# Kernel optimization log

Hardware: AMD Instinct MI355X
Metric: run time of the kernel (lower is better)

Reference implementation:

```python
import jax, jax.numpy as jnp
from jax import lax
import numpy as np

NUM_KIND = 4
V, H, B = 34, 32, 4096   # raw vertical (2 rows dropped), horizontal, batch
KS = 33                  # odd-rounded max(V-2, H)
NUM_DEPTH = 4
N_SQ = 100


def _conv(x, w):
    # x: (N,1,h,w), w: (1,1,KS,KS); torch Conv2d == cross-correlation == lax default
    return lax.conv_general_dilated(x, w, (1, 1), 'SAME',
                                    dimension_numbers=('NCHW', 'OIHW', 'NCHW'))


def _conv_k(x, w):
    # x: (K,B,1,h,w) -> conv each map with the shared 1-channel kernel
    k, b, c, h, wd = x.shape
    return _conv(x.reshape(k * b, c, h, wd), w).reshape(k, b, c, h, wd)


def setup_inputs() -> dict:
    key = jax.random.key(0)
    ks = jax.random.split(key, 8)
    std = 0.3
    return {
        'dots':    jax.random.randint(ks[0], (V, H, B), 0, NUM_KIND + 1, dtype=jnp.int32),
        'w_each':  jax.random.normal(ks[1], (1, 1, KS, KS), jnp.float32) * std,
        'w_not':   jax.random.normal(ks[2], (1, 1, KS, KS), jnp.float32) * std,
        'w_not2':  jax.random.normal(ks[3], (1, 1, KS, KS), jnp.float32) * std,
        'w_empty': jax.random.normal(ks[4], (1, 1, KS, KS), jnp.float32) * std,
        'W1':      jax.random.normal(ks[5], (N_SQ, (V - 2) * H), jnp.float32) * std,
        'W2':      jax.random.normal(ks[6], (N_SQ, N_SQ), jnp.float32) * std,
        'W3':      jax.random.normal(ks[7], (1, N_SQ), jnp.float32) * std,
    }


def reference(dots, w_each, w_not, w_not2, w_empty, W1, W2, W3):
    # drop last 2 vertical rows, layout (V-2,H,B) -> (B,1,V-2,H)
    board = dots[:-2].astype(jnp.float32).transpose(2, 0, 1)[:, None]  # (B,1,h,w)

    empty = (board == 0).astype(jnp.float32)
    E = _conv(empty, w_empty)                                           # (B,1,h,w)

    kinds = jnp.arange(1, NUM_KIND + 1, dtype=board.dtype).reshape(NUM_KIND, 1, 1, 1, 1)
    each = (board[None] == kinds).astype(jnp.float32)                   # (K,B,1,h,w)
    notm = ((each + empty[None]) == 0).astype(jnp.float32)              # (K,B,1,h,w)

    # first pass: per-color value, masked to that color's cells
    notm_conv = _conv_k(notm, w_not)      # note: the torch code LOGS the convolved not-mask
    v = _conv_k(each, w_each) + E[None] - notm_conv
    L = each * v                          # each_color_value_log (masked)
    s = jax.nn.sigmoid(L.sum(axis=0))     # all_color_value_2nd, (B,1,h,w)

    # iterative diffusion; torch mutates the log in-place each depth:
    # L <- mask * (L + E + conv2nd(notm_conv * before)); before is detached
    for _ in range(NUM_DEPTH):
        before = lax.stop_gradient(s)
        C = _conv_k(notm_conv * before[None], w_not2)
        L = each * (L + E[None] + C)
        s = jax.nn.sigmoid(L.sum(axis=0))

    feat = s.reshape(s.shape[0], -1)      # (B, (V-2)*H)
    x = jax.nn.leaky_relu(feat @ W1.T, 0.2)
    x = jax.nn.leaky_relu(x @ W2.T, 0.2)
    return x @ W3.T                        # (B,1)
```

## Files before the change

### kernel.cpp

```cpp
#include <hip/hip_runtime.h>
#include <cstdint>
#include <cstddef>


typedef _Float16 f16;
typedef __attribute__((ext_vector_type(8))) _Float16 f16x8;
typedef __attribute__((ext_vector_type(4))) float f32x4;

#define NB   4096
#define PIX  1024
#define MR   (NB * 4)

__device__ __forceinline__ void gld_lds16(const void* g, void* l) {
    __builtin_amdgcn_global_load_lds(
        (const __attribute__((address_space(1))) void*)g,
        (__attribute__((address_space(3))) void*)l, 16, 0, 0);
}

__global__ void build_all(const float* __restrict__ we, const float* __restrict__ wn,
                          const float* __restrict__ wn2, const float* __restrict__ wem,
                          const float* __restrict__ W1, const int* __restrict__ dots,
                          f16* __restrict__ Me, f16* __restrict__ Mn,
                          f16* __restrict__ Mn2, f16* __restrict__ Mem,
                          f16* __restrict__ W1b, unsigned char* __restrict__ board) {
    __shared__ unsigned char tile[64][68];
    int bi = blockIdx.x, t = threadIdx.x;
    if (bi < 4096) {
        int idx = bi * 256 + t;
        int o = idx >> 10, in = idx & 1023;
        int i = o >> 5, j = o & 31, a = in >> 5, b = in & 31;
        int u = a - i + 16, v = b - j + 16;
        bool ok = (u >= 0) && (u < 33) && (v >= 0) && (v < 33);
        int w = u * 33 + v;
        float ve = 0.f, vn = 0.f, vn2 = 0.f, vem = 0.f;
        if (ok) { ve = we[w]; vn = wn[w]; vn2 = wn2[w]; vem = wem[w]; }
        Me[idx]  = (f16)ve;
        Mn[idx]  = (f16)vn;
        Mn2[idx] = (f16)vn2;
        Mem[idx] = (f16)vem;
    } else if (bi < 4608) {
        int idx = (bi - 4096) * 256 + t;
        int j = idx >> 10, i = idx & 1023;
        W1b[idx] = (f16)(j < 100 ? W1[j * 1024 + i] : 0.f);
    } else {
        int bb = bi - 4608;
        int bp = bb & 15, bn = bb >> 4;
        int p0 = bp * 64, n0 = bn * 64;
        int ln = t & 63, lp = t >> 6;
#pragma unroll
        for (int j = 0; j < 16; j++) {
            int p = lp * 16 + j;
            tile[p][ln] = (unsigned char)dots[(size_t)(p0 + p) * 4096 + n0 + ln];
        }
        __syncthreads();
#pragma unroll
        for (int j = 0; j < 16; j++) {
            int n = lp * 16 + j;
            board[(size_t)(n0 + n) * 1024 + p0 + ln] = tile[ln][n];
        }
    }
}

template <int MODE, int ASRC>
__device__ __forceinline__ void run_gemm(
    int bjob, int ypx, int nx, char* smem,
    const f16* __restrict__ X, const f16* __restrict__ B,
    const unsigned char* __restrict__ board, const f16* __restrict__ En,
    const f16* __restrict__ NCs, f16* __restrict__ Lsel,
    f16* __restrict__ Pout, f16* __restrict__ outB, int ldo) {
    char* smB = smem;
    char* smA = smem + 16384;

    const int tid = threadIdx.x;
    const int wv = tid >> 6, ln = tid & 63;
    const int wm = wv >> 1, wn_ = wv & 1;
    const int lr = ln & 15, lq = ln >> 4;

    int xcd = bjob & 7, slot = bjob >> 3;
    int bx = slot % nx;
    int by = xcd * ypx + slot / nx;
    const int rtile = by * 128, otile = bx * 128;
    const int img0 = (ASRC == 4) ? rtile : (rtile >> 2);

    const f32x4 fz = {0.f, 0.f, 0.f, 0.f};
    f32x4 acc[4][4];
#pragma unroll
    for (int i = 0; i < 4; i++)
#pragma unroll
        for (int j = 0; j < 4; j++) acc[i][j] = fz;

    for (int kb = 0; kb < 1024; kb += 64) {
#pragma unroll
        for (int t = 0; t < 4; t++) {
            int c = (wv * 4 + t) * 64 + ln;
            int row = c >> 3, gcol = (c & 7) ^ (row & 7);
            gld_lds16(B + (size_t)(otile + row) * 1024 + kb + gcol * 8, smB + c * 16);
        }
        if (ASRC == 0) {
#pragma unroll
            for (int t = 0; t < 4; t++) {
                int c = (wv * 4 + t) * 64 + ln;
                int row = c >> 3, gcol = (c & 7) ^ (row & 7);
                gld_lds16(X + (size_t)(rtile + row) * 1024 + kb + gcol * 8, smA + c * 16);
            }
        } else if (ASRC == 4) {
#pragma unroll
            for (int t = 0; t < 2; t++) {
                int c = t * 256 + wv * 64 + ln;
                int row = c >> 2, g = (c & 3) ^ (row & 3);
                gld_lds16(board + (size_t)(img0 + row) * 1024 + kb + g * 16, smA + c * 16);
            }
        } else {
            if (wv < 2) {
                int c = wv * 64 + ln;
                int row = c >> 2, g = (c & 3) ^ (row & 3);
                gld_lds16(board + (size_t)(img0 + row) * 1024 + kb + g * 16, smA + c * 16);
            }
        }
        __syncthreads();

#pragma unroll
        for (int kk = 0; kk < 2; kk++) {
            const int oct = kk * 4 + lq;
            f16x8 af[4], bfr[4];
#pragma unroll
            for (int i = 0; i < 4; i++) {
                int rrow = wm * 64 + i * 16 + lr;
                if (ASRC == 0) {
                    af[i] = *(const f16x8*)(smA + rrow * 128 + (oct ^ (rrow & 7)) * 16);
                } else {
                    int m = (ASRC == 4) ? rrow : (rrow >> 2);
                    int k1 = (rrow & 3) + 1;
                    uint64_t bb = *(const uint64_t*)(smA + m * 64 +
                                    ((oct >> 1) ^ (m & 3)) * 16 + (oct & 1) * 8);
                    f16x8 v;
#pragma unroll
                    for (int jj = 0; jj < 8; jj++) {
                        int bj = (int)((bb >> (8 * jj)) & 0xff);
                        bool on = (ASRC == 2) ? (bj == k1)
                                : (ASRC == 3) ? (bj != 0 && bj != k1)
                                              : (bj == 0);
                        v[jj] = on ? (f16)1.f : (f16)0.f;
                    }
                    af[i] = v;
                }
            }
#pragma unroll
            for (int j = 0; j < 4; j++) {
                int brow = wn_ * 64 + j * 16 + lr;
                bfr[j] = *(const f16x8*)(smB + brow * 128 + (oct ^ (brow & 7)) * 16);
            }
#pragma unroll
            for (int i = 0; i < 4; i++)
#pragma unroll
                for (int j = 0; j < 4; j++)
                    acc[i][j] = __builtin_amdgcn_mfma_f32_16x16x32_f16(
                        af[i], bfr[j], acc[i][j], 0, 0, 0);
        }
        __syncthreads();
    }

#pragma unroll
    for (int i = 0; i < 4; i++) {
        int rbase = rtile + wm * 64 + i * 16 + lq * 4;
#pragma unroll
        for (int j = 0; j < 4; j++) {
            int o = otile + wn_ * 64 + j * 16 + lr;
            f32x4 a = acc[i][j];
            if (MODE == 0) {
#pragma unroll
                for (int v = 0; v < 4; v++)
                    outB[(size_t)(rbase + v) * ldo + o] = (f16)a[v];
            } else {
                int n = rbase >> 2;
                size_t no = (size_t)n * PIX + o;
                int c = board[no];
                float asel = (c == 1) ? a[0] : (c == 2) ? a[1] : (c == 3) ? a[2] : a[3];
                size_t r0 = (size_t)rbase * PIX + o;
                f16 nc0 = NCs[r0], nc1 = NCs[r0 + PIX];
                f16 nc2 = NCs[r0 + 2 * PIX], nc3 = NCs[r0 + 3 * PIX];
                float L = 0.f;
                if (c > 0) {
                    float ncsel = (float)((c == 1) ? nc0 : (c == 2) ? nc1
                                        : (c == 3) ? nc2 : nc3);
                    L = asel + (float)En[no] - ncsel;
                }
                Lsel[no] = (f16)L;
                f16 s = (f16)(1.f / (1.f + __expf(-L)));
                Pout[r0]           = nc0 * s;
                Pout[r0 + PIX]     = nc1 * s;
                Pout[r0 + 2 * PIX] = nc2 * s;
                Pout[r0 + 3 * PIX] = nc3 * s;
            }
        }
    }
}

__global__ void __launch_bounds__(256, 4) gemm_faA(
    const f16* __restrict__ Mn, const f16* __restrict__ Mem,
    const unsigned char* __restrict__ board,
    f16* __restrict__ NC, f16* __restrict__ En) {
    __shared__ __attribute__((aligned(16))) char smem[24576];
    int bi = blockIdx.x;
    if (bi < 1024) {
        run_gemm<0, 3>(bi, 16, 8, smem, nullptr, Mn, board, nullptr, nullptr,
                       nullptr, nullptr, NC, PIX);
    } else {
        run_gemm<0, 4>(bi - 1024, 4, 8, smem, nullptr, Mem, board, nullptr, nullptr,
                       nullptr, nullptr, En, PIX);
    }
}

__global__ void __launch_bounds__(256, 4) gemm_faB(
    const f16* __restrict__ Me, const unsigned char* __restrict__ board,
    const f16* __restrict__ En, const f16* __restrict__ NC,
    f16* __restrict__ Lsel, f16* __restrict__ P1) {
    __shared__ __attribute__((aligned(16))) char smem[24576];
    run_gemm<2, 2>(blockIdx.x, 16, 8, smem, nullptr, Me, board, En, NC,
                   Lsel, P1, nullptr, 0);
}

template <int MODE>
__global__ void __launch_bounds__(256, 2) gemm_depth(
    const f16* __restrict__ Pin, const f16* __restrict__ Mn2,
    const unsigned char* __restrict__ board, const f16* __restrict__ NC,
    const f16* __restrict__ En, f16* __restrict__ Lsel,
    f16* __restrict__ Pout, f16* __restrict__ feat) {
    __shared__ __attribute__((aligned(16))) char smem[32768];
    char* smB = smem;
    char* smA = smem + 16384;

    const int tid = threadIdx.x;
    const int wv = tid >> 6, ln = tid & 63;
    const int wm = wv >> 1, wn_ = wv & 1;
    const int lr = ln & 15, lq = ln >> 4;

    int bi = blockIdx.x;
    int xcd = bi & 7, slot = bi >> 3;
    int bx = slot & 7;
    int by = xcd * 16 + (slot >> 3);
    const int rtile = by * 128, otile = bx * 128;

    const f32x4 fz = {0.f, 0.f, 0.f, 0.f};
    f32x4 acc[4][4];
#pragma unroll
    for (int i = 0; i < 4; i++)
#pragma unroll
        for (int j = 0; j < 4; j++) acc[i][j] = fz;

    for (int kb = 0; kb < 1024; kb += 64) {
#pragma unroll
        for (int t = 0; t < 4; t++) {
            int c = (wv * 4 + t) * 64 + ln;
            int row = c >> 3, gcol = (c & 7) ^ (row & 7);
            gld_lds16(Mn2 + (size_t)(otile + row) * 1024 + kb + gcol * 8, smB + c * 16);
            gld_lds16(Pin + (size_t)(rtile + row) * 1024 + kb + gcol * 8, smA + c * 16);
        }
        __syncthreads();

#pragma unroll
        for (int kk = 0; kk < 2; kk++) {
            const int oct = kk * 4 + lq;
            f16x8 af[4], bfr[4];
#pragma unroll
            for (int i = 0; i < 4; i++) {
                int rrow = wm * 64 + i * 16 + lr;
                af[i] = *(const f16x8*)(smA + rrow * 128 + (oct ^ (rrow & 7)) * 16);
            }
#pragma unroll
            for (int j = 0; j < 4; j++) {
                int brow = wn_ * 64 + j * 16 + lr;
                bfr[j] = *(const f16x8*)(smB + brow * 128 + (oct ^ (brow & 7)) * 16);
            }
#pragma unroll
            for (int i = 0; i < 4; i++)
#pragma unroll
                for (int j = 0; j < 4; j++)
                    acc[i][j] = __builtin_amdgcn_mfma_f32_16x16x32_f16(
                        af[i], bfr[j], acc[i][j], 0, 0, 0);
        }
        __syncthreads();
    }

#pragma unroll
    for (int i = 0; i < 4; i++) {
        int rbase = rtile + wm * 64 + i * 16 + lq * 4;
#pragma unroll
        for (int j = 0; j < 4; j++) {
            int o = otile + wn_ * 64 + j * 16 + lr;
            f32x4 a = acc[i][j];
            int n = rbase >> 2;
            size_t no = (size_t)n * PIX + o;
            int c = board[no];
            float asel = (c == 1) ? a[0] : (c == 2) ? a[1] : (c == 3) ? a[2] : a[3];
            float E = (float)En[no];
            float Lnew = (c > 0) ? ((float)Lsel[no] + E + asel) : 0.f;
            float s = 1.f / (1.f + __expf(-Lnew));
            if (MODE == 4) {
                feat[no] = (f16)s;
            } else {
                Lsel[no] = (f16)Lnew;
                f16 sh = (f16)s;
                size_t r0 = (size_t)rbase * PIX + o;
                Pout[r0]           = NC[r0] * sh;
                Pout[r0 + PIX]     = NC[r0 + PIX] * sh;
                Pout[r0 + 2 * PIX] = NC[r0 + 2 * PIX] * sh;
                Pout[r0 + 3 * PIX] = NC[r0 + 3 * PIX] * sh;
            }
        }
    }
}

__global__ void __launch_bounds__(256) gemm_mlp_fused(
    const f16* __restrict__ feat, const f16* __restrict__ W1b,
    const float* __restrict__ W2, const float* __restrict__ W3,
    float* __restrict__ out) {
    __shared__ __attribute__((aligned(16))) char smem[47360];
    char* smB = smem;
    char* smA = smem + 16384;

    const int tid = threadIdx.x;
    const int wv = tid >> 6, ln = tid & 63;
    const int wm = wv >> 1, wn_ = wv & 1;
    const int lr = ln & 15, lq = ln >> 4;
    const int rtile = blockIdx.x * 128;

    const f32x4 fz = {0.f, 0.f, 0.f, 0.f};
    f32x4 acc[4][4];
#pragma unroll
    for (int i = 0; i < 4; i++)
#pragma unroll
        for (int j = 0; j < 4; j++) acc[i][j] = fz;

    for (int kb = 0; kb < 1024; kb += 64) {
#pragma unroll
        for (int t = 0; t < 4; t++) {
            int c = (wv * 4 + t) * 64 + ln;
            int row = c >> 3, gcol = (c & 7) ^ (row & 7);
            gld_lds16(W1b  + (size_t)row * 1024 + kb + gcol * 8, smB + c * 16);
            gld_lds16(feat + (size_t)(rtile + row) * 1024 + kb + gcol * 8, smA + c * 16);
        }
        __syncthreads();
#pragma unroll
        for (int kk = 0; kk < 2; kk++) {
            const int oct = kk * 4 + lq;
            f16x8 af[4], bfr[4];
#pragma unroll
            for (int i = 0; i < 4; i++) {
                int rrow = wm * 64 + i * 16 + lr;
                af[i] = *(const f16x8*)(smA + rrow * 128 + (oct ^ (rrow & 7)) * 16);
            }
#pragma unroll
            for (int j = 0; j < 4; j++) {
                int brow = wn_ * 64 + j * 16 + lr;
                bfr[j] = *(const f16x8*)(smB + brow * 128 + (oct ^ (brow & 7)) * 16);
            }
#pragma unroll
            for (int i = 0; i < 4; i++)
#pragma unroll
                for (int j = 0; j < 4; j++)
                    acc[i][j] = __builtin_amdgcn_mfma_f32_16x16x32_f16(
                        af[i], bfr[j], acc[i][j], 0, 0, 0);
        }
        __syncthreads();
    }

    float* xs  = (float*)smem;
    f16*   sW2 = (f16*)(smem + 25856);
    float* sW3 = (float*)(smem + 45856);
    float* red = (float*)(smem + 46272);
    for (int idx = tid; idx < 10000; idx += 256) sW2[idx] = (f16)W2[idx];
    if (tid < 100) sW3[tid] = W3[tid];

    for (int half = 0; half < 2; half++) {
        if (wm == half) {
#pragma unroll
            for (int i = 0; i < 4; i++) {
                int rb = i * 16 + lq * 4;
#pragma unroll
                for (int j = 0; j < 4; j++) {
                    int o = wn_ * 64 + j * 16 + lr;
                    if (o < 100) {
                        f32x4 a = acc[i][j];
#pragma unroll
                        for (int v = 0; v < 4; v++) {
                            float x = a[v];
                            xs[(rb + v) * 101 + o] = x > 0.f ? x : 0.2f * x;
                        }
                    }
                }
            }
        }
        __syncthreads();
        int nb = tid >> 2, q = tid & 3;
        const float* xrow = xs + nb * 101;
        float partial = 0.f;
        for (int jj = 0; jj < 25; jj++) {
            int j = q + jj * 4;
            const f16* w2r = sW2 + j * 100;
            float a2 = 0.f;
#pragma unroll
            for (int i = 0; i < 100; i++) a2 += (float)w2r[i] * xrow[i];
            partial += sW3[j] * (a2 > 0.f ? a2 : 0.2f * a2);
        }
        red[tid] = partial;
        __syncthreads();
        if (q == 0)
            out[rtile + half * 64 + nb] = red[tid] + red[tid + 1] + red[tid + 2] + red[tid + 3];
        __syncthreads();
    }
}

extern "C" void kernel_launch(void* const* d_in, const int* in_sizes, int n_in,
                              void* d_out, int out_size, void* d_ws, size_t ws_size,
                              hipStream_t stream) {
    (void)in_sizes; (void)n_in; (void)out_size; (void)ws_size;
    const int*   dots   = (const int*)d_in[0];
    const float* w_each = (const float*)d_in[1];
    const float* w_not  = (const float*)d_in[2];
    const float* w_not2 = (const float*)d_in[3];
    const float* w_emp  = (const float*)d_in[4];
    const float* W1 = (const float*)d_in[5];
    const float* W2 = (const float*)d_in[6];
    const float* W3 = (const float*)d_in[7];
    float* out = (float*)d_out;

    char* ws = (char*)d_ws;
    size_t off = 0;
    auto alloc = [&](size_t bytes) -> char* {
        char* p = ws + off;
        off += (bytes + 255) & ~(size_t)255;
        return p;
    };
    f16* Me    = (f16*)alloc((size_t)PIX * PIX * 2);
    f16* Mn    = (f16*)alloc((size_t)PIX * PIX * 2);
    f16* Mn2   = (f16*)alloc((size_t)PIX * PIX * 2);
    f16* Mem   = (f16*)alloc((size_t)PIX * PIX * 2);
    f16* W1b   = (f16*)alloc((size_t)128 * PIX * 2);
    unsigned char* board = (unsigned char*)alloc((size_t)NB * PIX);
    f16* NC    = (f16*)alloc((size_t)MR * PIX * 2);
    f16* En    = (f16*)alloc((size_t)NB * PIX * 2);
    f16* Pa    = (f16*)alloc((size_t)MR * PIX * 2);
    f16* Pb    = (f16*)alloc((size_t)MR * PIX * 2);
    f16* feat  = (f16*)alloc((size_t)NB * PIX * 2);
    f16* Lsel  = (f16*)alloc((size_t)NB * PIX * 2);

    dim3 blk(256);
    build_all<<<5632, blk, 0, stream>>>(w_each, w_not, w_not2, w_emp, W1, dots,
                                        Me, Mn, Mn2, Mem, W1b, board);
    gemm_faA<<<1280, blk, 0, stream>>>(Mn, Mem, board, NC, En);
    gemm_faB<<<1024, blk, 0, stream>>>(Me, board, En, NC, Lsel, Pa);
    gemm_depth<3><<<1024, blk, 0, stream>>>(Pa, Mn2, board, NC, En, Lsel, Pb, nullptr);
    gemm_depth<3><<<1024, blk, 0, stream>>>(Pb, Mn2, board, NC, En, Lsel, Pa, nullptr);
    gemm_depth<3><<<1024, blk, 0, stream>>>(Pa, Mn2, board, NC, En, Lsel, Pb, nullptr);
    gemm_depth<4><<<1024, blk, 0, stream>>>(Pb, Mn2, board, NC, En, Lsel, nullptr, feat);
    gemm_mlp_fused<<<32, blk, 0, stream>>>(feat, W1b, W2, W3, out);
}
```

Baseline: 409.4 us.

## Precompute f16 masks and fuse sigmoid-times-notconv product into depth GEMM operand load

Adds an expand_masks kernel that writes the per-kind each, not and empty masks as f16 matrices once, so the first-pass GEMMs load plain f16 A tiles instead of decoding board bytes per MFMA fragment. The depth GEMMs no longer read a precomputed P = NC*s buffer (4 values per pixel written in every epilogue). They load NC and the per-image sigmoid S tile into LDS and multiply them while building the A fragments. Each epilogue then writes only Lsel and S per pixel. The cost is extra mask buffers, the extra expansion pass, one more LDS tile and a vector multiply in the inner loop.

```diff
diff --git a/kernel.cpp b/kernel.cpp
--- a/kernel.cpp
+++ b/kernel.cpp
@@ -61,13 +61,43 @@
     }
 }
 
-template <int MODE, int ASRC>
+__global__ void expand_masks(const unsigned char* __restrict__ board,
+                             f16* __restrict__ eachF, f16* __restrict__ notmF,
+                             f16* __restrict__ emptyF) {
+    int bi = blockIdx.x, t = threadIdx.x;
+    if (bi < 8192) {
+        int idx = bi * 256 + t;
+        int r = idx >> 7, w0 = (idx & 127) << 3;
+        int n = r >> 2, k1 = (r & 3) + 1;
+        uint64_t bb = *(const uint64_t*)(board + (size_t)n * 1024 + w0);
+        f16x8 e, m;
+#pragma unroll
+        for (int j = 0; j < 8; j++) {
+            int bj = (int)((bb >> (8 * j)) & 0xff);
+            e[j] = (bj == k1) ? (f16)1.f : (f16)0.f;
+            m[j] = (bj != 0 && bj != k1) ? (f16)1.f : (f16)0.f;
+        }
+        *(f16x8*)(eachF + (size_t)idx * 8) = e;
+        *(f16x8*)(notmF + (size_t)idx * 8) = m;
+    } else {
+        int idx = (bi - 8192) * 256 + t;
+        int n = idx >> 7, w0 = (idx & 127) << 3;
+        uint64_t bb = *(const uint64_t*)(board + (size_t)n * 1024 + w0);
+        f16x8 e;
+#pragma unroll
+        for (int j = 0; j < 8; j++)
+            e[j] = (((bb >> (8 * j)) & 0xff) == 0) ? (f16)1.f : (f16)0.f;
+        *(f16x8*)(emptyF + (size_t)idx * 8) = e;
+    }
+}
+
+template <int MODE>
 __device__ __forceinline__ void run_gemm(
     int bjob, int ypx, int nx, char* smem,
     const f16* __restrict__ X, const f16* __restrict__ B,
     const unsigned char* __restrict__ board, const f16* __restrict__ En,
     const f16* __restrict__ NCs, f16* __restrict__ Lsel,
-    f16* __restrict__ Pout, f16* __restrict__ outB, int ldo) {
+    f16* __restrict__ Sout, f16* __restrict__ outB, int ldo) {
     char* smB = smem;
     char* smA = smem + 16384;
 
@@ -80,7 +110,6 @@
     int bx = slot % nx;
     int by = xcd * ypx + slot / nx;
     const int rtile = by * 128, otile = bx * 128;
-    const int img0 = (ASRC == 4) ? rtile : (rtile >> 2);
 
     const f32x4 fz = {0.f, 0.f, 0.f, 0.f};
     f32x4 acc[4][4];
@@ -95,27 +124,7 @@
             int c = (wv * 4 + t) * 64 + ln;
             int row = c >> 3, gcol = (c & 7) ^ (row & 7);
             gld_lds16(B + (size_t)(otile + row) * 1024 + kb + gcol * 8, smB + c * 16);
-        }
-        if (ASRC == 0) {
-#pragma unroll
-            for (int t = 0; t < 4; t++) {
-                int c = (wv * 4 + t) * 64 + ln;
-                int row = c >> 3, gcol = (c & 7) ^ (row & 7);
-                gld_lds16(X + (size_t)(rtile + row) * 1024 + kb + gcol * 8, smA + c * 16);
-            }
-        } else if (ASRC == 4) {
-#pragma unroll
-            for (int t = 0; t < 2; t++) {
-                int c = t * 256 + wv * 64 + ln;
-                int row = c >> 2, g = (c & 3) ^ (row & 3);
-                gld_lds16(board + (size_t)(img0 + row) * 1024 + kb + g * 16, smA + c * 16);
-            }
-        } else {
-            if (wv < 2) {
-                int c = wv * 64 + ln;
-                int row = c >> 2, g = (c & 3) ^ (row & 3);
-                gld_lds16(board + (size_t)(img0 + row) * 1024 + kb + g * 16, smA + c * 16);
-            }
+            gld_lds16(X + (size_t)(rtile + row) * 1024 + kb + gcol * 8, smA + c * 16);
         }
         __syncthreads();
 
@@ -126,24 +135,7 @@
 #pragma unroll
             for (int i = 0; i < 4; i++) {
                 int rrow = wm * 64 + i * 16 + lr;
-                if (ASRC == 0) {
-                    af[i] = *(const f16x8*)(smA + rrow * 128 + (oct ^ (rrow & 7)) * 16);
-                } else {
-                    int m = (ASRC == 4) ? rrow : (rrow >> 2);
-                    int k1 = (rrow & 3) + 1;
-                    uint64_t bb = *(const uint64_t*)(smA + m * 64 +
-                                    ((oct >> 1) ^ (m & 3)) * 16 + (oct & 1) * 8);
-                    f16x8 v;
-#pragma unroll
-                    for (int jj = 0; jj < 8; jj++) {
-                        int bj = (int)((bb >> (8 * jj)) & 0xff);
-                        bool on = (ASRC == 2) ? (bj == k1)
-                                : (ASRC == 3) ? (bj != 0 && bj != k1)
-                                              : (bj == 0);
-                        v[jj] = on ? (f16)1.f : (f16)0.f;
-                    }
-                    af[i] = v;
-                }
+                af[i] = *(const f16x8*)(smA + rrow * 128 + (oct ^ (rrow & 7)) * 16);
             }
 #pragma unroll
             for (int j = 0; j < 4; j++) {
@@ -175,22 +167,15 @@
                 int n = rbase >> 2;
                 size_t no = (size_t)n * PIX + o;
                 int c = board[no];
-                float asel = (c == 1) ? a[0] : (c == 2) ? a[1] : (c == 3) ? a[2] : a[3];
-                size_t r0 = (size_t)rbase * PIX + o;
-                f16 nc0 = NCs[r0], nc1 = NCs[r0 + PIX];
-                f16 nc2 = NCs[r0 + 2 * PIX], nc3 = NCs[r0 + 3 * PIX];
                 float L = 0.f;
                 if (c > 0) {
-                    float ncsel = (float)((c == 1) ? nc0 : (c == 2) ? nc1
-                                        : (c == 3) ? nc2 : nc3);
+                    float asel = (c == 1) ? a[0] : (c == 2) ? a[1]
+                               : (c == 3) ? a[2] : a[3];
+                    float ncsel = (float)NCs[(size_t)(rbase + c - 1) * PIX + o];
                     L = asel + (float)En[no] - ncsel;
                 }
                 Lsel[no] = (f16)L;
-                f16 s = (f16)(1.f / (1.f + __expf(-L)));
-                Pout[r0]           = nc0 * s;
-                Pout[r0 + PIX]     = nc1 * s;
-                Pout[r0 + 2 * PIX] = nc2 * s;
-                Pout[r0 + 3 * PIX] = nc3 * s;
+                Sout[no] = (f16)(1.f / (1.f + __expf(-L)));
             }
         }
     }
@@ -198,37 +183,37 @@
 
 __global__ void __launch_bounds__(256, 4) gemm_faA(
     const f16* __restrict__ Mn, const f16* __restrict__ Mem,
-    const unsigned char* __restrict__ board,
+    const f16* __restrict__ notmF, const f16* __restrict__ emptyF,
     f16* __restrict__ NC, f16* __restrict__ En) {
-    __shared__ __attribute__((aligned(16))) char smem[24576];
+    __shared__ __attribute__((aligned(16))) char smem[32768];
     int bi = blockIdx.x;
     if (bi < 1024) {
-        run_gemm<0, 3>(bi, 16, 8, smem, nullptr, Mn, board, nullptr, nullptr,
-                       nullptr, nullptr, NC, PIX);
+        run_gemm<0>(bi, 16, 8, smem, notmF, Mn, nullptr, nullptr,
+                    nullptr, nullptr, nullptr, NC, PIX);
     } else {
-        run_gemm<0, 4>(bi - 1024, 4, 8, smem, nullptr, Mem, board, nullptr, nullptr,
-                       nullptr, nullptr, En, PIX);
+        run_gemm<0>(bi - 1024, 4, 8, smem, emptyF, Mem, nullptr, nullptr,
+                    nullptr, nullptr, nullptr, En, PIX);
     }
 }
 
 __global__ void __launch_bounds__(256, 4) gemm_faB(
-    const f16* __restrict__ Me, const unsigned char* __restrict__ board,
-    const f16* __restrict__ En, const f16* __restrict__ NC,
-    f16* __restrict__ Lsel, f16* __restrict__ P1) {
-    __shared__ __attribute__((aligned(16))) char smem[24576];
-    run_gemm<2, 2>(blockIdx.x, 16, 8, smem, nullptr, Me, board, En, NC,
-                   Lsel, P1, nullptr, 0);
-}
-
-template <int MODE>
+    const f16* __restrict__ Me, const f16* __restrict__ eachF,
+    const unsigned char* __restrict__ board, const f16* __restrict__ En,
+    const f16* __restrict__ NC, f16* __restrict__ Lsel, f16* __restrict__ S1) {
+    __shared__ __attribute__((aligned(16))) char smem[32768];
+    run_gemm<2>(blockIdx.x, 16, 8, smem, eachF, Me, board, En, NC,
+                Lsel, S1, nullptr, 0);
+}
+
 __global__ void __launch_bounds__(256, 2) gemm_depth(
-    const f16* __restrict__ Pin, const f16* __restrict__ Mn2,
-    const unsigned char* __restrict__ board, const f16* __restrict__ NC,
-    const f16* __restrict__ En, f16* __restrict__ Lsel,
-    f16* __restrict__ Pout, f16* __restrict__ feat) {
-    __shared__ __attribute__((aligned(16))) char smem[32768];
+    const f16* __restrict__ NC, const f16* __restrict__ Mn2,
+    const unsigned char* __restrict__ board, const f16* __restrict__ En,
+    const f16* __restrict__ Sin, f16* __restrict__ Lsel,
+    f16* __restrict__ Sout) {
+    __shared__ __attribute__((aligned(16))) char smem[36864];
     char* smB = smem;
     char* smA = smem + 16384;
+    char* smS = smem + 32768;
 
     const int tid = threadIdx.x;
     const int wv = tid >> 6, ln = tid & 63;
@@ -240,6 +225,7 @@
     int bx = slot & 7;
     int by = xcd * 16 + (slot >> 3);
     const int rtile = by * 128, otile = bx * 128;
+    const int n0 = rtile >> 2;
 
     const f32x4 fz = {0.f, 0.f, 0.f, 0.f};
     f32x4 acc[4][4];
@@ -254,7 +240,11 @@
             int c = (wv * 4 + t) * 64 + ln;
             int row = c >> 3, gcol = (c & 7) ^ (row & 7);
             gld_lds16(Mn2 + (size_t)(otile + row) * 1024 + kb + gcol * 8, smB + c * 16);
-            gld_lds16(Pin + (size_t)(rtile + row) * 1024 + kb + gcol * 8, smA + c * 16);
+            gld_lds16(NC  + (size_t)(rtile + row) * 1024 + kb + gcol * 8, smA + c * 16);
+        }
+        {
+            int row = tid >> 3, col = tid & 7;
+            gld_lds16(Sin + (size_t)(n0 + row) * 1024 + kb + col * 8, smS + tid * 16);
         }
         __syncthreads();
 
@@ -265,7 +255,9 @@
 #pragma unroll
             for (int i = 0; i < 4; i++) {
                 int rrow = wm * 64 + i * 16 + lr;
-                af[i] = *(const f16x8*)(smA + rrow * 128 + (oct ^ (rrow & 7)) * 16);
+                f16x8 nv = *(const f16x8*)(smA + rrow * 128 + (oct ^ (rrow & 7)) * 16);
+                f16x8 sv = *(const f16x8*)(smS + (rrow >> 2) * 128 + oct * 16);
+                af[i] = nv * sv;
             }
 #pragma unroll
             for (int j = 0; j < 4; j++) {
@@ -292,21 +284,14 @@
             int n = rbase >> 2;
             size_t no = (size_t)n * PIX + o;
             int c = board[no];
-            float asel = (c == 1) ? a[0] : (c == 2) ? a[1] : (c == 3) ? a[2] : a[3];
-            float E = (float)En[no];
-            float Lnew = (c > 0) ? ((float)Lsel[no] + E + asel) : 0.f;
-            float s = 1.f / (1.f + __expf(-Lnew));
-            if (MODE == 4) {
-                feat[no] = (f16)s;
-            } else {
-                Lsel[no] = (f16)Lnew;
-                f16 sh = (f16)s;
-                size_t r0 = (size_t)rbase * PIX + o;
-                Pout[r0]           = NC[r0] * sh;
-                Pout[r0 + PIX]     = NC[r0 + PIX] * sh;
-                Pout[r0 + 2 * PIX] = NC[r0 + 2 * PIX] * sh;
-                Pout[r0 + 3 * PIX] = NC[r0 + 3 * PIX] * sh;
-            }
+            float Lnew = 0.f;
+            if (c > 0) {
+                float asel = (c == 1) ? a[0] : (c == 2) ? a[1]
+                           : (c == 3) ? a[2] : a[3];
+                Lnew = (float)Lsel[no] + (float)En[no] + asel;
+            }
+            Lsel[no] = (f16)Lnew;
+            Sout[no] = (f16)(1.f / (1.f + __expf(-Lnew)));
         }
     }
 }
@@ -438,21 +423,24 @@
     f16* Mem   = (f16*)alloc((size_t)PIX * PIX * 2);
     f16* W1b   = (f16*)alloc((size_t)128 * PIX * 2);
     unsigned char* board = (unsigned char*)alloc((size_t)NB * PIX);
+    f16* eachF = (f16*)alloc((size_t)MR * PIX * 2);
+    f16* notmF = (f16*)alloc((size_t)MR * PIX * 2);
+    f16* emptyF= (f16*)alloc((size_t)NB * PIX * 2);
     f16* NC    = (f16*)alloc((size_t)MR * PIX * 2);
     f16* En    = (f16*)alloc((size_t)NB * PIX * 2);
-    f16* Pa    = (f16*)alloc((size_t)MR * PIX * 2);
-    f16* Pb    = (f16*)alloc((size_t)MR * PIX * 2);
-    f16* feat  = (f16*)alloc((size_t)NB * PIX * 2);
     f16* Lsel  = (f16*)alloc((size_t)NB * PIX * 2);
+    f16* Sa    = (f16*)alloc((size_t)NB * PIX * 2);
+    f16* Sb    = (f16*)alloc((size_t)NB * PIX * 2);
 
     dim3 blk(256);
     build_all<<<5632, blk, 0, stream>>>(w_each, w_not, w_not2, w_emp, W1, dots,
                                         Me, Mn, Mn2, Mem, W1b, board);
-    gemm_faA<<<1280, blk, 0, stream>>>(Mn, Mem, board, NC, En);
-    gemm_faB<<<1024, blk, 0, stream>>>(Me, board, En, NC, Lsel, Pa);
-    gemm_depth<3><<<1024, blk, 0, stream>>>(Pa, Mn2, board, NC, En, Lsel, Pb, nullptr);
-    gemm_depth<3><<<1024, blk, 0, stream>>>(Pb, Mn2, board, NC, En, Lsel, Pa, nullptr);
-    gemm_depth<3><<<1024, blk, 0, stream>>>(Pa, Mn2, board, NC, En, Lsel, Pb, nullptr);
-    gemm_depth<4><<<1024, blk, 0, stream>>>(Pb, Mn2, board, NC, En, Lsel, nullptr, feat);
-    gemm_mlp_fused<<<32, blk, 0, stream>>>(feat, W1b, W2, W3, out);
-}
+    expand_masks<<<10240, blk, 0, stream>>>(board, eachF, notmF, emptyF);
+    gemm_faA<<<1280, blk, 0, stream>>>(Mn, Mem, notmF, emptyF, NC, En);
+    gemm_faB<<<1024, blk, 0, stream>>>(Me, eachF, board, En, NC, Lsel, Sa);
+    gemm_depth<<<1024, blk, 0, stream>>>(NC, Mn2, board, En, Sa, Lsel, Sb);
+    gemm_depth<<<1024, blk, 0, stream>>>(NC, Mn2, board, En, Sb, Lsel, Sa);
+    gemm_depth<<<1024, blk, 0, stream>>>(NC, Mn2, board, En, Sa, Lsel, Sb);
+    gemm_depth<<<1024, blk, 0, stream>>>(NC, Mn2, board, En, Sb, Lsel, Sa);
+    gemm_mlp_fused<<<32, blk, 0, stream>>>(Sa, W1b, W2, W3, out);
+}
```

Result: slower. 446.9 us (+9.2%).
